# Kernel optimization log

Measured on AMD Instinct MI355X. Metric: run time of the kernel, lower is better.

Reference implementation:

```python
import jax, jax.numpy as jnp
import numpy as np
import math

B, T, D, H = 2, 2048, 1024, 16
HD = D // H
SOFTMAX_EPS = 1e-9
LN_EPS = 1e-5
NEG_INF = -1e9

def setup_inputs() -> dict:
    key = jax.random.key(0)
    ks = jax.random.split(key, 8)
    x = jax.random.normal(ks[0], (B, T, D), dtype=jnp.float32)
    # additive causal mask: 0 on/below diagonal, -1e9 above
    causal = jnp.where(jnp.tril(jnp.ones((T, T), dtype=bool)), 0.0, NEG_INF).astype(jnp.float32)
    attn_mask = jnp.broadcast_to(causal, (B, T, T))
    s = 0.02
    W_proj = jax.random.normal(ks[1], (D, 3 * D), dtype=jnp.float32) * s
    b_proj = jnp.zeros((3 * D,), dtype=jnp.float32)
    W_out = jax.random.normal(ks[2], (D, D), dtype=jnp.float32) * s
    b_out = jnp.zeros((D,), dtype=jnp.float32)
    ln_gamma = jnp.ones((D,), dtype=jnp.float32)
    ln_beta = jnp.zeros((D,), dtype=jnp.float32)
    return {"x": x, "attn_mask": attn_mask, "W_proj": W_proj, "b_proj": b_proj,
            "W_out": W_out, "b_out": b_out, "ln_gamma": ln_gamma, "ln_beta": ln_beta}

def reference(x, attn_mask, W_proj, b_proj, W_out, b_out, ln_gamma, ln_beta):
    Bv, Tv = x.shape[0], x.shape[1]
    qkv = x @ W_proj + b_proj                      # [B,T,3D]
    q, k, v = jnp.split(qkv, 3, axis=-1)
    q = q.reshape(Bv, Tv, H, HD).transpose(0, 2, 1, 3)  # [B,H,T,hd]
    k = k.reshape(Bv, Tv, H, HD).transpose(0, 2, 1, 3)
    v = v.reshape(Bv, Tv, H, HD).transpose(0, 2, 1, 3)
    # NOTE: mask added BEFORE scaling, matching the original module
    scores = (jnp.einsum('bhqd,bhkd->bhqk', q, k) + attn_mask[:, None, :, :]) / math.sqrt(HD)
    num = jnp.exp(scores)
    wts = num / (num.sum(axis=-1, keepdims=True) + SOFTMAX_EPS)  # eps-safe softmax, no max-subtract
    attn = jnp.einsum('bhqk,bhkd->bhqd', wts, v)   # [B,H,T,hd]
    y = attn.transpose(0, 2, 1, 3).reshape(Bv, Tv, D)
    z = x + y @ W_out + b_out
    mu = z.mean(axis=-1, keepdims=True)
    var = ((z - mu) ** 2).mean(axis=-1, keepdims=True)
    return (z - mu) / jnp.sqrt(var + LN_EPS) * ln_gamma + ln_beta
```

## Files before the change

kernel.cpp:

```cpp
#include <hip/hip_runtime.h>
#include <stdint.h>

typedef unsigned short u16;
typedef __attribute__((ext_vector_type(8))) short short8;
typedef __attribute__((ext_vector_type(4))) short sh4;
typedef __attribute__((ext_vector_type(4))) float f32x4;

#define MFMA16(a,b,c) __builtin_amdgcn_mfma_f32_16x16x32_bf16((a),(b),(c),0,0,0)

__device__ __forceinline__ u16 f2bf(float f) {
  union { float f; uint32_t u; } c; c.f = f;
  uint32_t u = c.u;
  return (u16)((u + 0x7fffu + ((u >> 16) & 1u)) >> 16);
}

__device__ __forceinline__ void async_cp16(const void* g, void* l) {
  __builtin_amdgcn_global_load_lds((__attribute__((address_space(1))) void*)g,
                                   (__attribute__((address_space(3))) void*)l,
                                   16, 0, 0);
}

__global__ __launch_bounds__(256) void prep(const float* __restrict__ x,
                                            const float* __restrict__ Wp,
                                            const float* __restrict__ Wo,
                                            u16* __restrict__ x_bf,
                                            u16* __restrict__ WpT,
                                            u16* __restrict__ WoT) {
  __shared__ float tile[32][33];
  int bx = blockIdx.x;
  if (bx < 4096) {
    int i = bx * 256 + threadIdx.x;
    float4 v = ((const float4*)x)[i];
    ushort4 o; o.x = f2bf(v.x); o.y = f2bf(v.y); o.z = f2bf(v.z); o.w = f2bf(v.w);
    ((ushort4*)x_bf)[i] = o;
    return;
  }
  const float* in; u16* out; int C, blk;
  if (bx < 7168) { in = Wp; out = WpT; C = 3072; blk = bx - 4096; }
  else           { in = Wo; out = WoT; C = 1024; blk = bx - 7168; }
  const int R = 1024;
  int nbc = C >> 5;
  int c0 = (blk % nbc) << 5;
  int r0 = (blk / nbc) << 5;
  int tx = threadIdx.x & 31, ty = threadIdx.x >> 5;
  for (int i = 0; i < 32; i += 8)
    tile[ty + i][tx] = in[(size_t)(r0 + ty + i) * C + c0 + tx];
  __syncthreads();
  for (int i = 0; i < 32; i += 8)
    out[(size_t)(c0 + ty + i) * R + r0 + tx] = f2bf(tile[tx][ty + i]);
}

__global__ __launch_bounds__(256, 2) void gemm_qkv(
    const u16* __restrict__ A, const u16* __restrict__ Bt,
    const float* __restrict__ bias, u16* __restrict__ qkb, u16* __restrict__ Vtb) {
  __shared__ __align__(16) u16 As[4096];
  __shared__ __align__(16) u16 Bs[4096];
  int t = threadIdx.x;
  int w = t >> 6, lane = t & 63, quad = lane >> 4, l15 = lane & 15;
  int wr = w >> 1, wc = w & 1;
  int m0 = blockIdx.y * 128;
  int n0 = blockIdx.x * 128;
  bool isqk = (n0 < 2048);

  int c0 = t, c1 = t + 256;
  const u16* gA0 = A + (size_t)(m0 + (c0 >> 2)) * 1024 + ((c0 & 3) << 3);
  const u16* gA1 = A + (size_t)(m0 + (c1 >> 2)) * 1024 + ((c1 & 3) << 3);
  const u16* gB0 = Bt + (size_t)(n0 + (c0 >> 2)) * 1024 + ((c0 & 3) << 3);
  const u16* gB1 = Bt + (size_t)(n0 + (c1 >> 2)) * 1024 + ((c1 & 3) << 3);
  u16* lA0 = &As[c0 * 8]; u16* lA1 = &As[c1 * 8];
  u16* lB0 = &Bs[c0 * 8]; u16* lB1 = &Bs[c1 * 8];

  f32x4 acc[4][4];
  f32x4 zero = {0.f, 0.f, 0.f, 0.f};
  for (int mt = 0; mt < 4; mt++)
    for (int nt = 0; nt < 4; nt++) acc[mt][nt] = zero;

  for (int k0 = 0; k0 < 1024; k0 += 32) {
    __syncthreads();
    async_cp16(gA0 + k0, lA0);
    async_cp16(gA1 + k0, lA1);
    async_cp16(gB0 + k0, lB0);
    async_cp16(gB1 + k0, lB1);
    __syncthreads();
    short8 af[4], bf[4];
    for (int mt = 0; mt < 4; mt++)
      af[mt] = *(const short8*)&As[(wr * 64 + mt * 16 + l15) * 32 + quad * 8];
    for (int nt = 0; nt < 4; nt++)
      bf[nt] = *(const short8*)&Bs[(wc * 64 + nt * 16 + l15) * 32 + quad * 8];
    if (isqk) {
      for (int mt = 0; mt < 4; mt++)
        for (int nt = 0; nt < 4; nt++)
          acc[mt][nt] = MFMA16(bf[nt], af[mt], acc[mt][nt]);
    } else {
      for (int mt = 0; mt < 4; mt++)
        for (int nt = 0; nt < 4; nt++)
          acc[mt][nt] = MFMA16(af[mt], bf[nt], acc[mt][nt]);
    }
  }
  if (isqk) {
    for (int mt = 0; mt < 4; mt++) {
      int m = m0 + wr * 64 + mt * 16 + l15;
      for (int nt = 0; nt < 4; nt++) {
        int nb = n0 + wc * 64 + nt * 16 + quad * 4;
        float4 bv = *(const float4*)&bias[nb];
        ushort4 o;
        o.x = f2bf(acc[mt][nt][0] + bv.x);
        o.y = f2bf(acc[mt][nt][1] + bv.y);
        o.z = f2bf(acc[mt][nt][2] + bv.z);
        o.w = f2bf(acc[mt][nt][3] + bv.w);
        *(ushort4*)&qkb[(size_t)m * 2048 + nb] = o;
      }
    }
  } else {
    for (int nt = 0; nt < 4; nt++) {
      int n = n0 + wc * 64 + nt * 16 + l15;
      float bv = bias[n];
      int d = n - 2048;
      for (int mt = 0; mt < 4; mt++) {
        int mb = m0 + wr * 64 + mt * 16 + quad * 4;
        ushort4 o;
        o.x = f2bf(acc[mt][nt][0] + bv);
        o.y = f2bf(acc[mt][nt][1] + bv);
        o.z = f2bf(acc[mt][nt][2] + bv);
        o.w = f2bf(acc[mt][nt][3] + bv);
        *(ushort4*)&Vtb[(size_t)d * 4096 + mb] = o;
      }
    }
  }
}

__global__ __launch_bounds__(256, 2) void gemm_out_res(
    const u16* __restrict__ A, const u16* __restrict__ Bt,
    const float* __restrict__ bias, const float* __restrict__ X,
    float* __restrict__ Z) {
  __shared__ __align__(16) u16 As[4096];
  __shared__ __align__(16) u16 Bs[4096];
  int t = threadIdx.x;
  int w = t >> 6, lane = t & 63, quad = lane >> 4, l15 = lane & 15;
  int wr = w >> 1, wc = w & 1;
  int m0 = blockIdx.y * 128;
  int n0 = blockIdx.x * 128;

  int c0 = t, c1 = t + 256;
  const u16* gA0 = A + (size_t)(m0 + (c0 >> 2)) * 1024 + ((c0 & 3) << 3);
  const u16* gA1 = A + (size_t)(m0 + (c1 >> 2)) * 1024 + ((c1 & 3) << 3);
  const u16* gB0 = Bt + (size_t)(n0 + (c0 >> 2)) * 1024 + ((c0 & 3) << 3);
  const u16* gB1 = Bt + (size_t)(n0 + (c1 >> 2)) * 1024 + ((c1 & 3) << 3);
  u16* lA0 = &As[c0 * 8]; u16* lA1 = &As[c1 * 8];
  u16* lB0 = &Bs[c0 * 8]; u16* lB1 = &Bs[c1 * 8];

  f32x4 acc[4][4];
  f32x4 zero = {0.f, 0.f, 0.f, 0.f};
  for (int mt = 0; mt < 4; mt++)
    for (int nt = 0; nt < 4; nt++) acc[mt][nt] = zero;

  for (int k0 = 0; k0 < 1024; k0 += 32) {
    __syncthreads();
    async_cp16(gA0 + k0, lA0);
    async_cp16(gA1 + k0, lA1);
    async_cp16(gB0 + k0, lB0);
    async_cp16(gB1 + k0, lB1);
    __syncthreads();
    short8 af[4], bf[4];
    for (int mt = 0; mt < 4; mt++)
      af[mt] = *(const short8*)&As[(wr * 64 + mt * 16 + l15) * 32 + quad * 8];
    for (int nt = 0; nt < 4; nt++)
      bf[nt] = *(const short8*)&Bs[(wc * 64 + nt * 16 + l15) * 32 + quad * 8];
    for (int mt = 0; mt < 4; mt++)
      for (int nt = 0; nt < 4; nt++)
        acc[mt][nt] = MFMA16(bf[nt], af[mt], acc[mt][nt]);
  }
  for (int mt = 0; mt < 4; mt++) {
    int m = m0 + wr * 64 + mt * 16 + l15;
    for (int nt = 0; nt < 4; nt++) {
      int nb = n0 + wc * 64 + nt * 16 + quad * 4;
      float4 bv = *(const float4*)&bias[nb];
      size_t idx = (size_t)m * 1024 + nb;
      float4 xv = *(const float4*)&X[idx];
      float4 o;
      o.x = acc[mt][nt][0] + bv.x + xv.x;
      o.y = acc[mt][nt][1] + bv.y + xv.y;
      o.z = acc[mt][nt][2] + bv.z + xv.z;
      o.w = acc[mt][nt][3] + bv.w + xv.w;
      *(float4*)&Z[idx] = o;
    }
  }
}

#define LDP 68
__global__ __launch_bounds__(256, 2) void attn_v3(
    const u16* __restrict__ qk, const u16* __restrict__ Vt,
    u16* __restrict__ y) {
  __shared__ __align__(16) u16 K_lds[2][4096];
  __shared__ __align__(16) u16 V_lds[2][4096];
  __shared__ __align__(16) u16 P_lds[4 * 16 * LDP];
  int bx = blockIdx.x;
  int sub = bx >> 3;
  int bh = (bx & 7) * 4 + (sub >> 4);
  int slot = sub & 15;
  int h = bh & 15, b = bh >> 4;
  int t = threadIdx.x, w = t >> 6, lane = t & 63, quad = lane >> 4, l15 = lane & 15;
  size_t rowbase = (size_t)b * 2048;
  u16* Pw = P_lds + w * 16 * LDP;
  f32x4 zero = {0.f, 0.f, 0.f, 0.f};

  const u16 *Kg[2], *Vg[2];
  u16 *Kl[2][2], *Vl[2][2];
  for (int i = 0; i < 2; i++) {
    int c = t + 256 * i;
    int half = c >> 8, row = (c >> 2) & 63, cg = c & 3;
    int col = half * 32 + cg * 8;
    Kg[i] = qk + (rowbase + row) * 2048 + 1024 + h * 64 + col;
    Vg[i] = Vt + (size_t)(h * 64 + row) * 4096 + rowbase + col;
    Kl[0][i] = &K_lds[0][c * 8]; Kl[1][i] = &K_lds[1][c * 8];
    Vl[0][i] = &V_lds[0][c * 8]; Vl[1][i] = &V_lds[1][c * 8];
  }

  for (int i = 0; i < 2; i++) { async_cp16(Kg[i], Kl[0][i]); async_cp16(Vg[i], Vl[0][i]); }

  int cur = 0;
  for (int pass = 0; pass < 2; pass++) {
    int qt = pass ? (31 - slot) : slot;
    int q0 = qt * 64;
    short8 qf0, qf1;
    {
      const u16* qp = qk + (rowbase + q0 + w * 16 + l15) * 2048 + h * 64 + quad * 8;
      qf0 = *(const short8*)qp;
      qf1 = *(const short8*)(qp + 32);
    }
    f32x4 o[4];
    for (int nt = 0; nt < 4; nt++) o[nt] = zero;
    float rs[4] = {0.f, 0.f, 0.f, 0.f};

    for (int kt = 0; kt <= qt; kt++) {
      __syncthreads();
      int nxt = cur ^ 1;
      if (kt < qt) {
        size_t ko = (size_t)(kt + 1) * 64;
        for (int i = 0; i < 2; i++) {
          async_cp16(Kg[i] + ko * 2048, Kl[nxt][i]);
          async_cp16(Vg[i] + ko, Vl[nxt][i]);
        }
      } else if (pass == 0) {
        for (int i = 0; i < 2; i++) { async_cp16(Kg[i], Kl[nxt][i]); async_cp16(Vg[i], Vl[nxt][i]); }
      }
      const u16* Kb = K_lds[cur];
      const u16* Vb = V_lds[cur];
      f32x4 s[4];
      for (int nt = 0; nt < 4; nt++) {
        const u16* kr = Kb + (nt * 16 + l15) * 32 + quad * 8;
        f32x4 a2 = zero;
        a2 = MFMA16(qf0, *(const short8*)kr, a2);
        a2 = MFMA16(qf1, *(const short8*)(kr + 2048), a2);
        s[nt] = a2;
      }
      bool diag = (kt == qt);
      int qloc = w * 16 + quad * 4;
      for (int nt = 0; nt < 4; nt++) {
        int col = nt * 16 + l15;
        for (int r = 0; r < 4; r++) {
          float p = __expf(s[nt][r] * 0.125f);
          if (diag && col > qloc + r) p = 0.f;
          rs[r] += p;
          Pw[(quad * 4 + r) * LDP + col] = (u16)(__float_as_uint(p) >> 16);
        }
      }
      for (int c2 = 0; c2 < 2; c2++) {
        union { short8 v8; sh4 h2[2]; } u;
        u.h2[0] = *(const sh4*)&Pw[l15 * LDP + c2 * 32 + quad * 8];
        u.h2[1] = *(const sh4*)&Pw[l15 * LDP + c2 * 32 + quad * 8 + 4];
        for (int nt = 0; nt < 4; nt++) {
          const short8 bv = *(const short8*)&Vb[c2 * 2048 + (nt * 16 + l15) * 32 + quad * 8];
          o[nt] = MFMA16(u.v8, bv, o[nt]);
        }
      }
      cur = nxt;
    }
    for (int r = 0; r < 4; r++) {
      float v = rs[r];
      v += __shfl_xor(v, 1, 64);
      v += __shfl_xor(v, 2, 64);
      v += __shfl_xor(v, 4, 64);
      v += __shfl_xor(v, 8, 64);
      rs[r] = v;
    }
    for (int nt = 0; nt < 4; nt++) {
      for (int r = 0; r < 4; r++) {
        float ov = o[nt][r] / (rs[r] + 1e-9f);
        size_t qr = rowbase + q0 + w * 16 + quad * 4 + r;
        y[qr * 1024 + h * 64 + nt * 16 + l15] = f2bf(ov);
      }
    }
  }
}

__global__ __launch_bounds__(256) void ln_kernel(const float* __restrict__ Z,
                                                 const float* __restrict__ gamma,
                                                 const float* __restrict__ beta,
                                                 float* __restrict__ out) {
  int row = blockIdx.x;
  int t = threadIdx.x;
  float4 v = ((const float4*)(Z + (size_t)row * 1024))[t];
  float s = v.x + v.y + v.z + v.w;
  float s2 = v.x * v.x + v.y * v.y + v.z * v.z + v.w * v.w;
  for (int m = 1; m < 64; m <<= 1) {
    s += __shfl_xor(s, m, 64);
    s2 += __shfl_xor(s2, m, 64);
  }
  __shared__ float ss[4], ss2[4];
  int w = t >> 6;
  if ((t & 63) == 0) { ss[w] = s; ss2[w] = s2; }
  __syncthreads();
  s = ss[0] + ss[1] + ss[2] + ss[3];
  s2 = ss2[0] + ss2[1] + ss2[2] + ss2[3];
  float mu = s * (1.0f / 1024.0f);
  float var = s2 * (1.0f / 1024.0f) - mu * mu;
  float inv = rsqrtf(var + 1e-5f);
  float4 g = ((const float4*)gamma)[t];
  float4 bb = ((const float4*)beta)[t];
  float4 o;
  o.x = (v.x - mu) * inv * g.x + bb.x;
  o.y = (v.y - mu) * inv * g.y + bb.y;
  o.z = (v.z - mu) * inv * g.z + bb.z;
  o.w = (v.w - mu) * inv * g.w + bb.w;
  ((float4*)(out + (size_t)row * 1024))[t] = o;
}

extern "C" void kernel_launch(void* const* d_in, const int* in_sizes, int n_in,
                              void* d_out, int out_size, void* d_ws, size_t ws_size,
                              hipStream_t stream) {
  const float* x     = (const float*)d_in[0];
  const float* Wp    = (const float*)d_in[2];
  const float* bp    = (const float*)d_in[3];
  const float* Wo    = (const float*)d_in[4];
  const float* bo    = (const float*)d_in[5];
  const float* gamma = (const float*)d_in[6];
  const float* beta  = (const float*)d_in[7];
  float* out = (float*)d_out;

  char* ws = (char*)d_ws;
  u16*   x_bf = (u16*)(ws);
  u16*   WpT  = (u16*)(ws + 8388608);
  u16*   WoT  = (u16*)(ws + 14680064);
  u16*   qkb  = (u16*)(ws + 16777216);
  u16*   Vtb  = (u16*)(ws + 33554432);
  u16*   y    = (u16*)(ws + 41943040);
  float* z    = (float*)(ws + 50331648);

  prep<<<8192, 256, 0, stream>>>(x, Wp, Wo, x_bf, WpT, WoT);

  dim3 gqkv(24, 32);
  gemm_qkv<<<gqkv, 256, 0, stream>>>(x_bf, WpT, bp, qkb, Vtb);

  attn_v3<<<512, 256, 0, stream>>>(qkb, Vtb, y);

  dim3 go(8, 32);
  gemm_out_res<<<go, 256, 0, stream>>>(y, WoT, bo, x, z);

  ln_kernel<<<4096, 256, 0, stream>>>(z, gamma, beta, out);
}
```

Measured before the change: 231.5 us.

## Widen attention query tiles, double-buffer GEMM loads, vectorize weight transpose

The attention kernel now has each block handle 128 query rows as two 64-row subtiles. Each K/V tile loaded into LDS is reused for both subtiles, which halves K/V traffic per query row, and the grid drops from 512 to 256 blocks. Both GEMMs switch to double-buffered LDS so the next K-slice loads while MFMAs run on the current one, at the cost of twice the shared memory. The weight transpose in prep uses 64x64 tiles with float4 loads and ushort4 stores. The smaller attention grid lowers parallelism and per-CU occupancy, and the diagonal tile does some extra masked work.

```diff
diff --git a/kernel.cpp b/kernel.cpp
--- a/kernel.cpp
+++ b/kernel.cpp
@@ -26,35 +26,52 @@
                                             u16* __restrict__ x_bf,
                                             u16* __restrict__ WpT,
                                             u16* __restrict__ WoT) {
-  __shared__ float tile[32][33];
   int bx = blockIdx.x;
+  int t = threadIdx.x;
   if (bx < 4096) {
-    int i = bx * 256 + threadIdx.x;
+    int i = bx * 256 + t;
     float4 v = ((const float4*)x)[i];
     ushort4 o; o.x = f2bf(v.x); o.y = f2bf(v.y); o.z = f2bf(v.z); o.w = f2bf(v.w);
     ((ushort4*)x_bf)[i] = o;
     return;
   }
+  __shared__ float tile[64][65];
   const float* in; u16* out; int C, blk;
-  if (bx < 7168) { in = Wp; out = WpT; C = 3072; blk = bx - 4096; }
-  else           { in = Wo; out = WoT; C = 1024; blk = bx - 7168; }
+  blk = bx - 4096;
+  if (blk < 768) { in = Wp; out = WpT; C = 3072; }
+  else           { in = Wo; out = WoT; C = 1024; blk -= 768; }
   const int R = 1024;
-  int nbc = C >> 5;
-  int c0 = (blk % nbc) << 5;
-  int r0 = (blk / nbc) << 5;
-  int tx = threadIdx.x & 31, ty = threadIdx.x >> 5;
-  for (int i = 0; i < 32; i += 8)
-    tile[ty + i][tx] = in[(size_t)(r0 + ty + i) * C + c0 + tx];
+  int nbc = C >> 6;
+  int c0 = (blk % nbc) << 6;
+  int r0 = (blk / nbc) << 6;
+  int li = t & 15;
+  int hi = t >> 4;
+  for (int i = 0; i < 4; i++) {
+    int r = hi + (i << 4);
+    float4 v = *(const float4*)&in[(size_t)(r0 + r) * C + c0 + (li << 2)];
+    tile[r][(li << 2) + 0] = v.x;
+    tile[r][(li << 2) + 1] = v.y;
+    tile[r][(li << 2) + 2] = v.z;
+    tile[r][(li << 2) + 3] = v.w;
+  }
   __syncthreads();
-  for (int i = 0; i < 32; i += 8)
-    out[(size_t)(c0 + ty + i) * R + r0 + tx] = f2bf(tile[tx][ty + i]);
+  int rr4 = li << 2;
+  for (int i = 0; i < 4; i++) {
+    int col = hi + (i << 4);
+    ushort4 o;
+    o.x = f2bf(tile[rr4 + 0][col]);
+    o.y = f2bf(tile[rr4 + 1][col]);
+    o.z = f2bf(tile[rr4 + 2][col]);
+    o.w = f2bf(tile[rr4 + 3][col]);
+    *(ushort4*)&out[(size_t)(c0 + col) * R + r0 + rr4] = o;
+  }
 }
 
 __global__ __launch_bounds__(256, 2) void gemm_qkv(
     const u16* __restrict__ A, const u16* __restrict__ Bt,
     const float* __restrict__ bias, u16* __restrict__ qkb, u16* __restrict__ Vtb) {
-  __shared__ __align__(16) u16 As[4096];
-  __shared__ __align__(16) u16 Bs[4096];
+  __shared__ __align__(16) u16 As[2][4096];
+  __shared__ __align__(16) u16 Bs[2][4096];
   int t = threadIdx.x;
   int w = t >> 6, lane = t & 63, quad = lane >> 4, l15 = lane & 15;
   int wr = w >> 1, wc = w & 1;
@@ -67,26 +84,33 @@
   const u16* gA1 = A + (size_t)(m0 + (c1 >> 2)) * 1024 + ((c1 & 3) << 3);
   const u16* gB0 = Bt + (size_t)(n0 + (c0 >> 2)) * 1024 + ((c0 & 3) << 3);
   const u16* gB1 = Bt + (size_t)(n0 + (c1 >> 2)) * 1024 + ((c1 & 3) << 3);
-  u16* lA0 = &As[c0 * 8]; u16* lA1 = &As[c1 * 8];
-  u16* lB0 = &Bs[c0 * 8]; u16* lB1 = &Bs[c1 * 8];
 
   f32x4 acc[4][4];
   f32x4 zero = {0.f, 0.f, 0.f, 0.f};
   for (int mt = 0; mt < 4; mt++)
     for (int nt = 0; nt < 4; nt++) acc[mt][nt] = zero;
 
+  async_cp16(gA0, &As[0][c0 * 8]);
+  async_cp16(gA1, &As[0][c1 * 8]);
+  async_cp16(gB0, &Bs[0][c0 * 8]);
+  async_cp16(gB1, &Bs[0][c1 * 8]);
+
+  int cur = 0;
   for (int k0 = 0; k0 < 1024; k0 += 32) {
     __syncthreads();
-    async_cp16(gA0 + k0, lA0);
-    async_cp16(gA1 + k0, lA1);
-    async_cp16(gB0 + k0, lB0);
-    async_cp16(gB1 + k0, lB1);
-    __syncthreads();
+    int nxt = cur ^ 1;
+    if (k0 + 32 < 1024) {
+      int k1 = k0 + 32;
+      async_cp16(gA0 + k1, &As[nxt][c0 * 8]);
+      async_cp16(gA1 + k1, &As[nxt][c1 * 8]);
+      async_cp16(gB0 + k1, &Bs[nxt][c0 * 8]);
+      async_cp16(gB1 + k1, &Bs[nxt][c1 * 8]);
+    }
     short8 af[4], bf[4];
     for (int mt = 0; mt < 4; mt++)
-      af[mt] = *(const short8*)&As[(wr * 64 + mt * 16 + l15) * 32 + quad * 8];
+      af[mt] = *(const short8*)&As[cur][(wr * 64 + mt * 16 + l15) * 32 + quad * 8];
     for (int nt = 0; nt < 4; nt++)
-      bf[nt] = *(const short8*)&Bs[(wc * 64 + nt * 16 + l15) * 32 + quad * 8];
+      bf[nt] = *(const short8*)&Bs[cur][(wc * 64 + nt * 16 + l15) * 32 + quad * 8];
     if (isqk) {
       for (int mt = 0; mt < 4; mt++)
         for (int nt = 0; nt < 4; nt++)
@@ -96,6 +120,7 @@
         for (int nt = 0; nt < 4; nt++)
           acc[mt][nt] = MFMA16(af[mt], bf[nt], acc[mt][nt]);
     }
+    cur = nxt;
   }
   if (isqk) {
     for (int mt = 0; mt < 4; mt++) {
@@ -133,8 +158,8 @@
     const u16* __restrict__ A, const u16* __restrict__ Bt,
     const float* __restrict__ bias, const float* __restrict__ X,
     float* __restrict__ Z) {
-  __shared__ __align__(16) u16 As[4096];
-  __shared__ __align__(16) u16 Bs[4096];
+  __shared__ __align__(16) u16 As[2][4096];
+  __shared__ __align__(16) u16 Bs[2][4096];
   int t = threadIdx.x;
   int w = t >> 6, lane = t & 63, quad = lane >> 4, l15 = lane & 15;
   int wr = w >> 1, wc = w & 1;
@@ -146,29 +171,37 @@
   const u16* gA1 = A + (size_t)(m0 + (c1 >> 2)) * 1024 + ((c1 & 3) << 3);
   const u16* gB0 = Bt + (size_t)(n0 + (c0 >> 2)) * 1024 + ((c0 & 3) << 3);
   const u16* gB1 = Bt + (size_t)(n0 + (c1 >> 2)) * 1024 + ((c1 & 3) << 3);
-  u16* lA0 = &As[c0 * 8]; u16* lA1 = &As[c1 * 8];
-  u16* lB0 = &Bs[c0 * 8]; u16* lB1 = &Bs[c1 * 8];
 
   f32x4 acc[4][4];
   f32x4 zero = {0.f, 0.f, 0.f, 0.f};
   for (int mt = 0; mt < 4; mt++)
     for (int nt = 0; nt < 4; nt++) acc[mt][nt] = zero;
 
+  async_cp16(gA0, &As[0][c0 * 8]);
+  async_cp16(gA1, &As[0][c1 * 8]);
+  async_cp16(gB0, &Bs[0][c0 * 8]);
+  async_cp16(gB1, &Bs[0][c1 * 8]);
+
+  int cur = 0;
   for (int k0 = 0; k0 < 1024; k0 += 32) {
     __syncthreads();
-    async_cp16(gA0 + k0, lA0);
-    async_cp16(gA1 + k0, lA1);
-    async_cp16(gB0 + k0, lB0);
-    async_cp16(gB1 + k0, lB1);
-    __syncthreads();
+    int nxt = cur ^ 1;
+    if (k0 + 32 < 1024) {
+      int k1 = k0 + 32;
+      async_cp16(gA0 + k1, &As[nxt][c0 * 8]);
+      async_cp16(gA1 + k1, &As[nxt][c1 * 8]);
+      async_cp16(gB0 + k1, &Bs[nxt][c0 * 8]);
+      async_cp16(gB1 + k1, &Bs[nxt][c1 * 8]);
+    }
     short8 af[4], bf[4];
     for (int mt = 0; mt < 4; mt++)
-      af[mt] = *(const short8*)&As[(wr * 64 + mt * 16 + l15) * 32 + quad * 8];
+      af[mt] = *(const short8*)&As[cur][(wr * 64 + mt * 16 + l15) * 32 + quad * 8];
     for (int nt = 0; nt < 4; nt++)
-      bf[nt] = *(const short8*)&Bs[(wc * 64 + nt * 16 + l15) * 32 + quad * 8];
+      bf[nt] = *(const short8*)&Bs[cur][(wc * 64 + nt * 16 + l15) * 32 + quad * 8];
     for (int mt = 0; mt < 4; mt++)
       for (int nt = 0; nt < 4; nt++)
         acc[mt][nt] = MFMA16(bf[nt], af[mt], acc[mt][nt]);
+    cur = nxt;
   }
   for (int mt = 0; mt < 4; mt++) {
     int m = m0 + wr * 64 + mt * 16 + l15;
@@ -188,107 +221,117 @@
 }
 
 #define LDP 68
-__global__ __launch_bounds__(256, 2) void attn_v3(
+__global__ __launch_bounds__(256, 2) void attn_v4(
     const u16* __restrict__ qk, const u16* __restrict__ Vt,
     u16* __restrict__ y) {
   __shared__ __align__(16) u16 K_lds[2][4096];
   __shared__ __align__(16) u16 V_lds[2][4096];
-  __shared__ __align__(16) u16 P_lds[4 * 16 * LDP];
+  __shared__ __align__(16) u16 P_lds[4 * 32 * LDP];
   int bx = blockIdx.x;
   int sub = bx >> 3;
-  int bh = (bx & 7) * 4 + (sub >> 4);
-  int slot = sub & 15;
+  int bh = (bx & 7) * 4 + (sub >> 3);
+  int slot = sub & 7;
   int h = bh & 15, b = bh >> 4;
   int t = threadIdx.x, w = t >> 6, lane = t & 63, quad = lane >> 4, l15 = lane & 15;
   size_t rowbase = (size_t)b * 2048;
-  u16* Pw = P_lds + w * 16 * LDP;
+  u16* Pw = P_lds + w * 32 * LDP;
   f32x4 zero = {0.f, 0.f, 0.f, 0.f};
 
   const u16 *Kg[2], *Vg[2];
-  u16 *Kl[2][2], *Vl[2][2];
   for (int i = 0; i < 2; i++) {
     int c = t + 256 * i;
     int half = c >> 8, row = (c >> 2) & 63, cg = c & 3;
     int col = half * 32 + cg * 8;
     Kg[i] = qk + (rowbase + row) * 2048 + 1024 + h * 64 + col;
     Vg[i] = Vt + (size_t)(h * 64 + row) * 4096 + rowbase + col;
-    Kl[0][i] = &K_lds[0][c * 8]; Kl[1][i] = &K_lds[1][c * 8];
-    Vl[0][i] = &V_lds[0][c * 8]; Vl[1][i] = &V_lds[1][c * 8];
-  }
-
-  for (int i = 0; i < 2; i++) { async_cp16(Kg[i], Kl[0][i]); async_cp16(Vg[i], Vl[0][i]); }
+  }
+  int cc0 = t * 8, cc1 = (t + 256) * 8;
+
+  async_cp16(Kg[0], &K_lds[0][cc0]); async_cp16(Kg[1], &K_lds[0][cc1]);
+  async_cp16(Vg[0], &V_lds[0][cc0]); async_cp16(Vg[1], &V_lds[0][cc1]);
 
   int cur = 0;
   for (int pass = 0; pass < 2; pass++) {
-    int qt = pass ? (31 - slot) : slot;
-    int q0 = qt * 64;
-    short8 qf0, qf1;
-    {
-      const u16* qp = qk + (rowbase + q0 + w * 16 + l15) * 2048 + h * 64 + quad * 8;
-      qf0 = *(const short8*)qp;
-      qf1 = *(const short8*)(qp + 32);
-    }
-    f32x4 o[4];
-    for (int nt = 0; nt < 4; nt++) o[nt] = zero;
-    float rs[4] = {0.f, 0.f, 0.f, 0.f};
-
-    for (int kt = 0; kt <= qt; kt++) {
+    int qt = pass ? (15 - slot) : slot;
+    int q0 = qt * 128;
+    int ktmax = 2 * qt + 1;
+    short8 qf[2][2];
+    for (int mt = 0; mt < 2; mt++) {
+      const u16* qp = qk + (rowbase + q0 + mt * 64 + w * 16 + l15) * 2048 + h * 64 + quad * 8;
+      qf[mt][0] = *(const short8*)qp;
+      qf[mt][1] = *(const short8*)(qp + 32);
+    }
+    f32x4 o[2][4];
+    for (int mt = 0; mt < 2; mt++)
+      for (int nt = 0; nt < 4; nt++) o[mt][nt] = zero;
+    float rs[2][4] = {{0.f, 0.f, 0.f, 0.f}, {0.f, 0.f, 0.f, 0.f}};
+
+    for (int kt = 0; kt <= ktmax; kt++) {
       __syncthreads();
       int nxt = cur ^ 1;
-      if (kt < qt) {
+      if (kt < ktmax) {
         size_t ko = (size_t)(kt + 1) * 64;
-        for (int i = 0; i < 2; i++) {
-          async_cp16(Kg[i] + ko * 2048, Kl[nxt][i]);
-          async_cp16(Vg[i] + ko, Vl[nxt][i]);
-        }
+        async_cp16(Kg[0] + ko * 2048, &K_lds[nxt][cc0]);
+        async_cp16(Kg[1] + ko * 2048, &K_lds[nxt][cc1]);
+        async_cp16(Vg[0] + ko, &V_lds[nxt][cc0]);
+        async_cp16(Vg[1] + ko, &V_lds[nxt][cc1]);
       } else if (pass == 0) {
-        for (int i = 0; i < 2; i++) { async_cp16(Kg[i], Kl[nxt][i]); async_cp16(Vg[i], Vl[nxt][i]); }
+        async_cp16(Kg[0], &K_lds[nxt][cc0]); async_cp16(Kg[1], &K_lds[nxt][cc1]);
+        async_cp16(Vg[0], &V_lds[nxt][cc0]); async_cp16(Vg[1], &V_lds[nxt][cc1]);
       }
       const u16* Kb = K_lds[cur];
       const u16* Vb = V_lds[cur];
-      f32x4 s[4];
+      for (int mt = 0; mt < 2; mt++) {
+        f32x4 s[4];
+        for (int nt = 0; nt < 4; nt++) {
+          const u16* kr = Kb + (nt * 16 + l15) * 32 + quad * 8;
+          f32x4 a2 = zero;
+          a2 = MFMA16(qf[mt][0], *(const short8*)kr, a2);
+          a2 = MFMA16(qf[mt][1], *(const short8*)(kr + 2048), a2);
+          s[nt] = a2;
+        }
+        bool gate = (kt >= 2 * qt + mt);
+        int qrow = q0 + mt * 64 + w * 16 + quad * 4;
+        int kbase = kt * 64;
+        for (int nt = 0; nt < 4; nt++) {
+          int col = kbase + nt * 16 + l15;
+          for (int r = 0; r < 4; r++) {
+            float p = __expf(s[nt][r] * 0.125f);
+            if (gate && col > qrow + r) p = 0.f;
+            rs[mt][r] += p;
+            Pw[(mt * 16 + quad * 4 + r) * LDP + nt * 16 + l15] =
+                (u16)(__float_as_uint(p) >> 16);
+          }
+        }
+      }
+      for (int c2 = 0; c2 < 2; c2++) {
+        for (int mt = 0; mt < 2; mt++) {
+          union { short8 v8; sh4 h2[2]; } u;
+          u.h2[0] = *(const sh4*)&Pw[(mt * 16 + l15) * LDP + c2 * 32 + quad * 8];
+          u.h2[1] = *(const sh4*)&Pw[(mt * 16 + l15) * LDP + c2 * 32 + quad * 8 + 4];
+          for (int nt = 0; nt < 4; nt++) {
+            const short8 bv = *(const short8*)&Vb[c2 * 2048 + (nt * 16 + l15) * 32 + quad * 8];
+            o[mt][nt] = MFMA16(u.v8, bv, o[mt][nt]);
+          }
+        }
+      }
+      cur = nxt;
+    }
+    for (int mt = 0; mt < 2; mt++) {
+      for (int r = 0; r < 4; r++) {
+        float v = rs[mt][r];
+        v += __shfl_xor(v, 1, 64);
+        v += __shfl_xor(v, 2, 64);
+        v += __shfl_xor(v, 4, 64);
+        v += __shfl_xor(v, 8, 64);
+        rs[mt][r] = v;
+      }
       for (int nt = 0; nt < 4; nt++) {
-        const u16* kr = Kb + (nt * 16 + l15) * 32 + quad * 8;
-        f32x4 a2 = zero;
-        a2 = MFMA16(qf0, *(const short8*)kr, a2);
-        a2 = MFMA16(qf1, *(const short8*)(kr + 2048), a2);
-        s[nt] = a2;
-      }
-      bool diag = (kt == qt);
-      int qloc = w * 16 + quad * 4;
-      for (int nt = 0; nt < 4; nt++) {
-        int col = nt * 16 + l15;
         for (int r = 0; r < 4; r++) {
-          float p = __expf(s[nt][r] * 0.125f);
-          if (diag && col > qloc + r) p = 0.f;
-          rs[r] += p;
-          Pw[(quad * 4 + r) * LDP + col] = (u16)(__float_as_uint(p) >> 16);
+          float ov = o[mt][nt][r] / (rs[mt][r] + 1e-9f);
+          size_t qr = rowbase + q0 + mt * 64 + w * 16 + quad * 4 + r;
+          y[qr * 1024 + h * 64 + nt * 16 + l15] = f2bf(ov);
         }
-      }
-      for (int c2 = 0; c2 < 2; c2++) {
-        union { short8 v8; sh4 h2[2]; } u;
-        u.h2[0] = *(const sh4*)&Pw[l15 * LDP + c2 * 32 + quad * 8];
-        u.h2[1] = *(const sh4*)&Pw[l15 * LDP + c2 * 32 + quad * 8 + 4];
-        for (int nt = 0; nt < 4; nt++) {
-          const short8 bv = *(const short8*)&Vb[c2 * 2048 + (nt * 16 + l15) * 32 + quad * 8];
-          o[nt] = MFMA16(u.v8, bv, o[nt]);
-        }
-      }
-      cur = nxt;
-    }
-    for (int r = 0; r < 4; r++) {
-      float v = rs[r];
-      v += __shfl_xor(v, 1, 64);
-      v += __shfl_xor(v, 2, 64);
-      v += __shfl_xor(v, 4, 64);
-      v += __shfl_xor(v, 8, 64);
-      rs[r] = v;
-    }
-    for (int nt = 0; nt < 4; nt++) {
-      for (int r = 0; r < 4; r++) {
-        float ov = o[nt][r] / (rs[r] + 1e-9f);
-        size_t qr = rowbase + q0 + w * 16 + quad * 4 + r;
-        y[qr * 1024 + h * 64 + nt * 16 + l15] = f2bf(ov);
       }
     }
   }
@@ -347,12 +390,12 @@
   u16*   y    = (u16*)(ws + 41943040);
   float* z    = (float*)(ws + 50331648);
 
-  prep<<<8192, 256, 0, stream>>>(x, Wp, Wo, x_bf, WpT, WoT);
+  prep<<<5120, 256, 0, stream>>>(x, Wp, Wo, x_bf, WpT, WoT);
 
   dim3 gqkv(24, 32);
   gemm_qkv<<<gqkv, 256, 0, stream>>>(x_bf, WpT, bp, qkb, Vtb);
 
-  attn_v3<<<512, 256, 0, stream>>>(qkb, Vtb, y);
+  attn_v4<<<256, 256, 0, stream>>>(qkb, Vtb, y);
 
   dim3 go(8, 32);
   gemm_out_res<<<go, 256, 0, stream>>>(y, WoT, bo, x, z);
```

Result: slower. 246.7 us (+6.5%).
